# Kernel optimization log

Hardware: AMD Instinct MI355X
Metric: run time of the kernel (lower is better)

Reference implementation:

```python
import jax, jax.numpy as jnp
import numpy as np
from jax import lax

B, T, I, H, L = 64, 256, 512, 1024, 2


def setup_inputs() -> dict:
    key = jax.random.key(0)
    ks = jax.random.split(key, 6)
    s = 0.05  # small init scale for numerical stability
    return {
        "x": jax.random.normal(ks[0], (B, T, I), dtype=jnp.float32),
        "h0": jnp.zeros((L, B, H), dtype=jnp.float32),
        "c0": jnp.zeros((L, B, H), dtype=jnp.float32),
        "W_ih_0": jax.random.normal(ks[1], (I, 4 * H), dtype=jnp.float32) * s,
        "W_hh_0": jax.random.normal(ks[2], (H, 4 * H), dtype=jnp.float32) * s,
        "b_0": jnp.zeros((4 * H,), dtype=jnp.float32),
        "W_ih_1": jax.random.normal(ks[3], (H, 4 * H), dtype=jnp.float32) * s,
        "W_hh_1": jax.random.normal(ks[4], (H, 4 * H), dtype=jnp.float32) * s,
        "b_1": jnp.zeros((4 * H,), dtype=jnp.float32),
    }


def _lstm_layer(x_tbd, h0, c0, W_ih, W_hh, b):
    """x_tbd: [T, B, in]; returns ([T, B, H], h_T, c_T). Standard (Zaremba) LSTM cell."""
    def step(carry, xt):
        h, c = carry
        gates = xt @ W_ih + h @ W_hh + b  # [B, 4H]
        i, f, g, o = jnp.split(gates, 4, axis=-1)
        i = jax.nn.sigmoid(i)
        f = jax.nn.sigmoid(f)
        g = jnp.tanh(g)
        o = jax.nn.sigmoid(o)
        c_new = f * c + i * g
        h_new = o * jnp.tanh(c_new)
        return (h_new, c_new), h_new

    (h_T, c_T), ys = lax.scan(step, (h0, c0), x_tbd)
    return ys, h_T, c_T


def reference(x, h0, c0, W_ih_0, W_hh_0, b_0, W_ih_1, W_hh_1, b_1):
    # x: [B, T, I] batch-first as in the torch module; scan over time.
    xt = jnp.swapaxes(x, 0, 1)  # [T, B, I]
    weights = [(W_ih_0, W_hh_0, b_0), (W_ih_1, W_hh_1, b_1)]
    hs, cs = [], []
    values = xt
    for l in range(L):
        W_ih, W_hh, b = weights[l]
        values, h_T, c_T = _lstm_layer(values, h0[l], c0[l], W_ih, W_hh, b)
        hs.append(h_T)
        cs.append(c_T)
    outputs = jnp.swapaxes(values, 0, 1)  # [B, T, H]
    return outputs, jnp.stack(hs, 0), jnp.stack(cs, 0)
```

## Files before the change

kernel.cpp:

```cpp
#include <hip/hip_runtime.h>
#include <hip/hip_bf16.h>

typedef __attribute__((ext_vector_type(8))) short short8;
typedef __attribute__((ext_vector_type(4))) float f32x4;

constexpr int BB = 64;
constexpr int TT = 256;
constexpr int II = 512;
constexpr int HH = 1024;

constexpr int NBLK = 256;
constexpr int NTHR = 512;

constexpr int HTILE = (HH / 8) * BB * 8;
constexpr int XTILE = (II / 8) * BB * 8;

constexpr size_t OFF_FLAGS = 0;
constexpr size_t OFF_WIH0T = 4096;
constexpr size_t OFF_WHH0T = OFF_WIH0T + (size_t)4096 * 512 * 2;
constexpr size_t OFF_WIH1T = OFF_WHH0T + (size_t)4096 * 1024 * 2;
constexpr size_t OFF_WHH1T = OFF_WIH1T + (size_t)4096 * 1024 * 2;
constexpr size_t OFF_XT    = OFF_WHH1T + (size_t)4096 * 1024 * 2;
constexpr size_t OFF_H0D   = OFF_XT + (size_t)TT * XTILE * 2;
constexpr size_t OFF_H1D   = OFF_H0D + (size_t)4 * HTILE * 2;

__device__ __forceinline__ float sigmoid_(float x) {
  return 1.f / (1.f + __expf(-x));
}
__device__ __forceinline__ float tanh_(float x) {
  float ax = fabsf(x);
  float e = __expf(-2.f * ax);
  float t = (1.f - e) / (1.f + e);
  return copysignf(t, x);
}

__global__ void zero_flags(int* f) { f[blockIdx.x * 256 + threadIdx.x] = 0; }

__global__ void transpose_to_bf16(const float* __restrict__ src,
                                  __hip_bfloat16* __restrict__ dst,
                                  int K, int N) {
  __shared__ float tile[64][65];
  const int n0 = blockIdx.x * 64;
  const int k0 = blockIdx.y * 64;
  const int tx = threadIdx.x & 63;
  const int ty = threadIdx.x >> 6;
#pragma unroll
  for (int i = 0; i < 64; i += 4)
    tile[ty + i][tx] = src[(size_t)(k0 + ty + i) * N + n0 + tx];
  __syncthreads();
#pragma unroll
  for (int i = 0; i < 64; i += 4) {
    const int n = ty + i;
    dst[(size_t)(n0 + n) * K + k0 + tx] = __float2bfloat16(tile[tx][n]);
  }
}

__global__ void tile_x(const float* __restrict__ x, __hip_bfloat16* __restrict__ xt) {
  const int t = blockIdx.x;
  const int k = threadIdx.x;
  __hip_bfloat16* o = xt + (size_t)t * XTILE;
  for (int b = 0; b < BB; ++b) {
    float v = x[((size_t)b * TT + t) * II + k];
    o[(k >> 3) * (BB * 8) + b * 8 + (k & 7)] = __float2bfloat16(v);
  }
}

__global__ void init_h(const float* __restrict__ h0, __hip_bfloat16* h0d, __hip_bfloat16* h1d) {
  const int idx = blockIdx.x * 256 + threadIdx.x;
  const int l = idx >> 16;
  const int b = (idx >> 10) & 63;
  const int j = idx & 1023;
  __hip_bfloat16 v = __float2bfloat16(h0[idx]);
  __hip_bfloat16* dst = l ? h1d : h0d;
  dst[(j >> 3) * (BB * 8) + b * 8 + (j & 7)] = v;
}

template <int KI, int KW, int LAYER>
__device__ __forceinline__ void scan_impl(
    const __hip_bfloat16* __restrict__ xsrc,
    const __hip_bfloat16* __restrict__ WiT,
    const __hip_bfloat16* __restrict__ WhT,
    const float* __restrict__ bias,
    const float* __restrict__ c0_in,
    __hip_bfloat16* h0d, __hip_bfloat16* h1d,
    float* __restrict__ out, int* flags, float (*part)[2][4][4][65],
    int bhalf, int jbase, bool leader) {
  const int tid = threadIdx.x;
  const int wave = tid >> 6;
  const int lane = tid & 63;
  const int cc = lane & 15;
  const int lrow = lane >> 4;

  const int kbase = wave * (KW * 32);

  short8 Bf[KW][4];
#pragma unroll
  for (int w = 0; w < KW; ++w) {
    const int kg = kbase + w * 32 + lrow * 8;
#pragma unroll
    for (int g = 0; g < 4; ++g) {
      const int gcol = g * HH + jbase + cc;
      const __hip_bfloat16* p;
      if (kg < KI) p = WiT + (size_t)gcol * KI + kg;
      else         p = WhT + (size_t)gcol * HH + (kg - KI);
      Bf[w][g] = *(const short8*)p;
    }
  }

  const int ejl = tid & 15;
  const int ebl = tid >> 4;
  const int ej = jbase + ejl;
  const int eb = bhalf * 32 + ebl;
  const int pm = ebl >> 4, psub = (ebl >> 2) & 3, pr = ebl & 3;
  const int plane = psub * 16 + ejl;
  const float bi = bias[ej];
  const float bf_ = bias[HH + ej];
  const float bg = bias[2 * HH + ej];
  const float bo = bias[3 * HH + ej];
  float cst = c0_in[(size_t)LAYER * BB * HH + (size_t)eb * HH + ej];

  for (int tau = 0; tau <= TT; ++tau) {
    if (tau > 0 && wave == 0) {
      for (;;) {
        int v0 = __hip_atomic_load(&flags[lane],       __ATOMIC_RELAXED, __HIP_MEMORY_SCOPE_AGENT);
        int v1 = __hip_atomic_load(&flags[lane + 64],  __ATOMIC_RELAXED, __HIP_MEMORY_SCOPE_AGENT);
        int v2 = __hip_atomic_load(&flags[lane + 128], __ATOMIC_RELAXED, __HIP_MEMORY_SCOPE_AGENT);
        int v3 = __hip_atomic_load(&flags[lane + 192], __ATOMIC_RELAXED, __HIP_MEMORY_SCOPE_AGENT);
        int mn = min(min(v0, v1), min(v2, v3));
        if (__all(mn >= tau)) break;
        __builtin_amdgcn_s_sleep(2);
      }
    }
    __syncthreads();
    asm volatile("s_waitcnt vmcnt(0)" ::: "memory");
    if (leader && wave == 0)
      __builtin_amdgcn_fence(__ATOMIC_ACQUIRE, "agent");
    asm volatile("buffer_inv sc0" ::: "memory");
    __builtin_amdgcn_sched_barrier(0);

    const bool active = (LAYER == 0) ? (tau < TT) : (tau >= 1);
    if (active) {
      const int p = (LAYER == 0) ? tau : tau - 1;
      const __hip_bfloat16* px;
      const __hip_bfloat16* ph;
      __hip_bfloat16* hout;
      if constexpr (LAYER == 0) {
        px = xsrc + (size_t)p * XTILE;
        ph = h0d + (size_t)(p & 3) * HTILE;
        hout = h0d + (size_t)((p + 1) & 3) * HTILE;
      } else {
        px = h0d + (size_t)((p + 1) & 3) * HTILE;
        ph = h1d + (size_t)(p & 3) * HTILE;
        hout = h1d + (size_t)((p + 1) & 3) * HTILE;
      }

      f32x4 acc[2][4] = {};
      short8 abuf[4][2];

      auto issue_pair = [&](int w, short8* dst) {
        const int kg = kbase + w * 32;
        const __hip_bfloat16* ab;
        int kc;
        bool hpath;
        if (kg < KI) { ab = px; kc = (kg >> 3) + lrow; hpath = (LAYER == 1); }
        else         { ab = ph; kc = ((kg - KI) >> 3) + lrow; hpath = true; }
#pragma unroll
        for (int m = 0; m < 2; ++m) {
          const __hip_bfloat16* ptr =
              ab + (size_t)kc * (BB * 8) + (size_t)(bhalf * 32 + m * 16 + cc) * 8;
          if (hpath)
            asm volatile("global_load_dwordx4 %0, %1, off sc0" : "=v"(dst[m]) : "v"(ptr));
          else
            asm volatile("global_load_dwordx4 %0, %1, off" : "=v"(dst[m]) : "v"(ptr));
        }
      };

#pragma unroll
      for (int w = 0; w < 4; ++w) issue_pair(w, abuf[w]);

#pragma unroll
      for (int w = 0; w < KW; ++w) {
        const int op = (KW - w < 4) ? (KW - w) : 4;
        const int vm = 2 * (op - 1);
        if (vm == 6)      asm volatile("s_waitcnt vmcnt(6)" ::: "memory");
        else if (vm == 4) asm volatile("s_waitcnt vmcnt(4)" ::: "memory");
        else if (vm == 2) asm volatile("s_waitcnt vmcnt(2)" ::: "memory");
        else              asm volatile("s_waitcnt vmcnt(0)" ::: "memory");
        __builtin_amdgcn_sched_barrier(0);
#pragma unroll
        for (int m = 0; m < 2; ++m)
#pragma unroll
          for (int g = 0; g < 4; ++g)
            acc[m][g] = __builtin_amdgcn_mfma_f32_16x16x32_bf16(
                abuf[w & 3][m], Bf[w][g], acc[m][g], 0, 0, 0);
        if (w + 4 < KW) issue_pair(w + 4, abuf[w & 3]);
      }

#pragma unroll
      for (int m = 0; m < 2; ++m)
#pragma unroll
        for (int g = 0; g < 4; ++g)
#pragma unroll
          for (int r = 0; r < 4; ++r)
            part[wave][m][g][r][lane] = acc[m][g][r];
      __syncthreads();

      float s0 = 0.f, s1 = 0.f, s2 = 0.f, s3 = 0.f;
#pragma unroll
      for (int w = 0; w < 8; ++w) {
        s0 += part[w][pm][0][pr][plane];
        s1 += part[w][pm][1][pr][plane];
        s2 += part[w][pm][2][pr][plane];
        s3 += part[w][pm][3][pr][plane];
      }
      float iv = sigmoid_(s0 + bi);
      float fv = sigmoid_(s1 + bf_);
      float gv = tanh_(s2 + bg);
      float ov = sigmoid_(s3 + bo);
      float cn = fv * cst + iv * gv;
      cst = cn;
      float hv = ov * tanh_(cn);
      __hip_bfloat16 hb = __float2bfloat16(hv);
      unsigned short hu = *reinterpret_cast<unsigned short*>(&hb);
      unsigned pu = (unsigned)__shfl_xor((int)hu, 1);
      if ((tid & 1) == 0) {
        uint32_t packed = (uint32_t)hu | ((pu & 0xffffu) << 16);
        uint32_t* hq = (uint32_t*)hout;
        __hip_atomic_store(hq + (ej >> 3) * 256 + eb * 4 + ((ej & 7) >> 1), packed,
                           __ATOMIC_RELAXED, __HIP_MEMORY_SCOPE_AGENT);
      }
      asm volatile("s_waitcnt vmcnt(0)" ::: "memory");
      __syncthreads();
      if (tid == 0)
        __hip_atomic_store(&flags[blockIdx.x], tau + 1, __ATOMIC_RELAXED, __HIP_MEMORY_SCOPE_AGENT);
      if constexpr (LAYER == 1)
        out[((size_t)eb * TT + p) * HH + ej] = hv;
      if (p == TT - 1) {
        out[(size_t)BB * TT * HH + (size_t)LAYER * BB * HH + (size_t)eb * HH + ej] = hv;
        out[(size_t)BB * TT * HH + (size_t)2 * BB * HH + (size_t)LAYER * BB * HH + (size_t)eb * HH + ej] = cn;
      }
    } else {
      __syncthreads();
      if (tid == 0)
        __hip_atomic_store(&flags[blockIdx.x], tau + 1, __ATOMIC_RELAXED, __HIP_MEMORY_SCOPE_AGENT);
    }
  }
}

__global__ __launch_bounds__(NTHR, 2) void lstm_scan(
    const __hip_bfloat16* __restrict__ xt,
    const __hip_bfloat16* __restrict__ Wih0T, const __hip_bfloat16* __restrict__ Whh0T,
    const __hip_bfloat16* __restrict__ Wih1T, const __hip_bfloat16* __restrict__ Whh1T,
    const float* __restrict__ b0, const float* __restrict__ b1,
    const float* __restrict__ c0_in,
    __hip_bfloat16* h0d, __hip_bfloat16* h1d,
    float* __restrict__ out, int* flags) {
  __shared__ float part[8][2][4][4][65];
  __shared__ int s_leader;
  if (threadIdx.x == 0) {
    unsigned xcd;
    asm volatile("s_getreg_b32 %0, hwreg(HW_REG_XCC_ID)" : "=s"(xcd));
    int t = __hip_atomic_fetch_add(&flags[256 + (xcd & 15)], 1,
                                   __ATOMIC_RELAXED, __HIP_MEMORY_SCOPE_AGENT);
    s_leader = (t == 0);
  }
  __syncthreads();
  const bool leader = (s_leader != 0);

  const int blk = blockIdx.x;
  const int jslot = blk & 63;
  const int bhalf = (blk >> 6) & 1;
  const int jbase = jslot * 16;
  if ((blk >> 7) == 0)
    scan_impl<512, 6, 0>(xt, Wih0T, Whh0T, b0, c0_in, h0d, h1d, out, flags, part, bhalf, jbase, leader);
  else
    scan_impl<1024, 8, 1>(nullptr, Wih1T, Whh1T, b1, c0_in, h0d, h1d, out, flags, part, bhalf, jbase, leader);
}

extern "C" void kernel_launch(void* const* d_in, const int* in_sizes, int n_in,
                              void* d_out, int out_size, void* d_ws, size_t ws_size,
                              hipStream_t stream) {
  (void)in_sizes; (void)n_in; (void)out_size; (void)ws_size;
  const float* x    = (const float*)d_in[0];
  const float* h0   = (const float*)d_in[1];
  const float* c0   = (const float*)d_in[2];
  const float* Wih0 = (const float*)d_in[3];
  const float* Whh0 = (const float*)d_in[4];
  const float* b0   = (const float*)d_in[5];
  const float* Wih1 = (const float*)d_in[6];
  const float* Whh1 = (const float*)d_in[7];
  const float* b1   = (const float*)d_in[8];
  float* out = (float*)d_out;
  char* ws = (char*)d_ws;

  int* flags = (int*)(ws + OFF_FLAGS);
  __hip_bfloat16* wih0t = (__hip_bfloat16*)(ws + OFF_WIH0T);
  __hip_bfloat16* whh0t = (__hip_bfloat16*)(ws + OFF_WHH0T);
  __hip_bfloat16* wih1t = (__hip_bfloat16*)(ws + OFF_WIH1T);
  __hip_bfloat16* whh1t = (__hip_bfloat16*)(ws + OFF_WHH1T);
  __hip_bfloat16* xtl   = (__hip_bfloat16*)(ws + OFF_XT);
  __hip_bfloat16* h0d   = (__hip_bfloat16*)(ws + OFF_H0D);
  __hip_bfloat16* h1d   = (__hip_bfloat16*)(ws + OFF_H1D);

  zero_flags<<<2, 256, 0, stream>>>(flags);
  transpose_to_bf16<<<dim3(64, 8),  256, 0, stream>>>(Wih0, wih0t, 512, 4096);
  transpose_to_bf16<<<dim3(64, 16), 256, 0, stream>>>(Whh0, whh0t, 1024, 4096);
  transpose_to_bf16<<<dim3(64, 16), 256, 0, stream>>>(Wih1, wih1t, 1024, 4096);
  transpose_to_bf16<<<dim3(64, 16), 256, 0, stream>>>(Whh1, whh1t, 1024, 4096);
  tile_x<<<TT, 512, 0, stream>>>(x, xtl);
  init_h<<<512, 256, 0, stream>>>(h0, h0d, h1d);
  lstm_scan<<<NBLK, NTHR, 0, stream>>>(xtl, wih0t, whh0t, wih1t, whh1t,
                                       b0, b1, c0, h0d, h1d, out, flags);
}
```

Before: 1.682 ms.

## Prefetch and compute dependency-free GEMM chunks before the per-step flag wait

Reorders each wave's K chunks so that the part of the gate GEMM not depending on the current step's recurrent state is loaded and multiplied before spinning on the inter-block flags. For layer 0 that part is the x input; for layer 1 it is the layer-0 output. Layer 1 now lags layer 0 by two steps and the h ring grows from 4 to 8 slots so that input is already published. It also drops the per-XCD leader election and explicit buffer_inv and sc0 loads, using an agent-scope acquire fence from wave 0 in every block instead. Hiding the input half of the GEMM behind the barrier latency targets the serial critical path. The costs are one extra pipeline step, an extra __syncthreads per step, and reliance on the fence alone for cache coherence.

After: 1.618 ms. 3.8% less time.

```diff
diff --git a/kernel.cpp b/kernel.cpp
--- a/kernel.cpp
+++ b/kernel.cpp
@@ -14,6 +14,7 @@
 
 constexpr int HTILE = (HH / 8) * BB * 8;
 constexpr int XTILE = (II / 8) * BB * 8;
+constexpr int RING = 8;
 
 constexpr size_t OFF_FLAGS = 0;
 constexpr size_t OFF_WIH0T = 4096;
@@ -22,7 +23,7 @@
 constexpr size_t OFF_WHH1T = OFF_WIH1T + (size_t)4096 * 1024 * 2;
 constexpr size_t OFF_XT    = OFF_WHH1T + (size_t)4096 * 1024 * 2;
 constexpr size_t OFF_H0D   = OFF_XT + (size_t)TT * XTILE * 2;
-constexpr size_t OFF_H1D   = OFF_H0D + (size_t)4 * HTILE * 2;
+constexpr size_t OFF_H1D   = OFF_H0D + (size_t)RING * HTILE * 2;
 
 __device__ __forceinline__ float sigmoid_(float x) {
   return 1.f / (1.f + __expf(-x));
@@ -75,7 +76,15 @@
   dst[(j >> 3) * (BB * 8) + b * 8 + (j & 7)] = v;
 }
 
-template <int KI, int KW, int LAYER>
+template <int LAYER>
+__device__ __forceinline__ int chunk_kg(int wave, int c) {
+  if constexpr (LAYER == 0)
+    return (c < 2) ? (wave * 2 + c) * 32 : 512 + (wave * 4 + (c - 2)) * 32;
+  else
+    return (c < 4) ? (wave * 4 + c) * 32 : 1024 + (wave * 4 + (c - 4)) * 32;
+}
+
+template <int KI, int KW, int CA, int LAYER>
 __device__ __forceinline__ void scan_impl(
     const __hip_bfloat16* __restrict__ xsrc,
     const __hip_bfloat16* __restrict__ WiT,
@@ -84,26 +93,24 @@
     const float* __restrict__ c0_in,
     __hip_bfloat16* h0d, __hip_bfloat16* h1d,
     float* __restrict__ out, int* flags, float (*part)[2][4][4][65],
-    int bhalf, int jbase, bool leader) {
+    int bhalf, int jbase) {
   const int tid = threadIdx.x;
   const int wave = tid >> 6;
   const int lane = tid & 63;
   const int cc = lane & 15;
   const int lrow = lane >> 4;
 
-  const int kbase = wave * (KW * 32);
-
   short8 Bf[KW][4];
 #pragma unroll
-  for (int w = 0; w < KW; ++w) {
-    const int kg = kbase + w * 32 + lrow * 8;
+  for (int c = 0; c < KW; ++c) {
+    const int kg = chunk_kg<LAYER>(wave, c) + lrow * 8;
 #pragma unroll
     for (int g = 0; g < 4; ++g) {
       const int gcol = g * HH + jbase + cc;
       const __hip_bfloat16* p;
       if (kg < KI) p = WiT + (size_t)gcol * KI + kg;
       else         p = WhT + (size_t)gcol * HH + (kg - KI);
-      Bf[w][g] = *(const short8*)p;
+      Bf[c][g] = *(const short8*)p;
     }
   }
 
@@ -119,7 +126,45 @@
   const float bo = bias[3 * HH + ej];
   float cst = c0_in[(size_t)LAYER * BB * HH + (size_t)eb * HH + ej];
 
-  for (int tau = 0; tau <= TT; ++tau) {
+  for (int tau = 0; tau < TT + 2; ++tau) {
+    const bool active = (LAYER == 0) ? (tau < TT) : (tau >= 2);
+    const int p = (LAYER == 0) ? tau : tau - 2;
+
+    const __hip_bfloat16* px;
+    const __hip_bfloat16* ph;
+    __hip_bfloat16* hout;
+    if constexpr (LAYER == 0) {
+      px = xsrc + (size_t)p * XTILE;
+      ph = h0d + (size_t)(p & (RING - 1)) * HTILE;
+      hout = h0d + (size_t)((p + 1) & (RING - 1)) * HTILE;
+    } else {
+      px = h0d + (size_t)((p + 1) & (RING - 1)) * HTILE;
+      ph = h1d + (size_t)(p & (RING - 1)) * HTILE;
+      hout = h1d + (size_t)((p + 1) & (RING - 1)) * HTILE;
+    }
+
+    f32x4 acc[2][4] = {};
+    short8 abuf[4][2];
+
+    auto issue_chunk = [&](int c, short8* dst) {
+      const int kg = chunk_kg<LAYER>(wave, c);
+      const __hip_bfloat16* ab;
+      int kc;
+      if (kg < KI) { ab = px; kc = (kg >> 3) + lrow; }
+      else         { ab = ph; kc = ((kg - KI) >> 3) + lrow; }
+#pragma unroll
+      for (int m = 0; m < 2; ++m) {
+        const __hip_bfloat16* ptr =
+            ab + (size_t)kc * (BB * 8) + (size_t)(bhalf * 32 + m * 16 + cc) * 8;
+        asm volatile("global_load_dwordx4 %0, %1, off" : "=v"(dst[m]) : "v"(ptr));
+      }
+    };
+
+    if (active) {
+#pragma unroll
+      for (int c = 0; c < CA; ++c) issue_chunk(c, abuf[c]);
+    }
+
     if (tau > 0 && wave == 0) {
       for (;;) {
         int v0 = __hip_atomic_load(&flags[lane],       __ATOMIC_RELAXED, __HIP_MEMORY_SCOPE_AGENT);
@@ -131,57 +176,32 @@
         __builtin_amdgcn_s_sleep(2);
       }
     }
+
+    if (active) {
+      asm volatile("s_waitcnt vmcnt(0)" ::: "memory");
+      __builtin_amdgcn_sched_barrier(0);
+#pragma unroll
+      for (int c = 0; c < CA; ++c)
+#pragma unroll
+        for (int m = 0; m < 2; ++m)
+#pragma unroll
+          for (int g = 0; g < 4; ++g)
+            acc[m][g] = __builtin_amdgcn_mfma_f32_16x16x32_bf16(
+                abuf[c][m], Bf[c][g], acc[m][g], 0, 0, 0);
+    }
+
     __syncthreads();
-    asm volatile("s_waitcnt vmcnt(0)" ::: "memory");
-    if (leader && wave == 0)
+    if (wave == 0)
       __builtin_amdgcn_fence(__ATOMIC_ACQUIRE, "agent");
-    asm volatile("buffer_inv sc0" ::: "memory");
-    __builtin_amdgcn_sched_barrier(0);
-
-    const bool active = (LAYER == 0) ? (tau < TT) : (tau >= 1);
+    __syncthreads();
+
     if (active) {
-      const int p = (LAYER == 0) ? tau : tau - 1;
-      const __hip_bfloat16* px;
-      const __hip_bfloat16* ph;
-      __hip_bfloat16* hout;
-      if constexpr (LAYER == 0) {
-        px = xsrc + (size_t)p * XTILE;
-        ph = h0d + (size_t)(p & 3) * HTILE;
-        hout = h0d + (size_t)((p + 1) & 3) * HTILE;
-      } else {
-        px = h0d + (size_t)((p + 1) & 3) * HTILE;
-        ph = h1d + (size_t)(p & 3) * HTILE;
-        hout = h1d + (size_t)((p + 1) & 3) * HTILE;
-      }
-
-      f32x4 acc[2][4] = {};
-      short8 abuf[4][2];
-
-      auto issue_pair = [&](int w, short8* dst) {
-        const int kg = kbase + w * 32;
-        const __hip_bfloat16* ab;
-        int kc;
-        bool hpath;
-        if (kg < KI) { ab = px; kc = (kg >> 3) + lrow; hpath = (LAYER == 1); }
-        else         { ab = ph; kc = ((kg - KI) >> 3) + lrow; hpath = true; }
-#pragma unroll
-        for (int m = 0; m < 2; ++m) {
-          const __hip_bfloat16* ptr =
-              ab + (size_t)kc * (BB * 8) + (size_t)(bhalf * 32 + m * 16 + cc) * 8;
-          if (hpath)
-            asm volatile("global_load_dwordx4 %0, %1, off sc0" : "=v"(dst[m]) : "v"(ptr));
-          else
-            asm volatile("global_load_dwordx4 %0, %1, off" : "=v"(dst[m]) : "v"(ptr));
-        }
-      };
-
-#pragma unroll
-      for (int w = 0; w < 4; ++w) issue_pair(w, abuf[w]);
-
-#pragma unroll
-      for (int w = 0; w < KW; ++w) {
-        const int op = (KW - w < 4) ? (KW - w) : 4;
-        const int vm = 2 * (op - 1);
+      constexpr int NB = KW - CA;
+#pragma unroll
+      for (int c = 0; c < NB; ++c) issue_chunk(CA + c, abuf[c]);
+#pragma unroll
+      for (int c = 0; c < NB; ++c) {
+        const int vm = 2 * (NB - 1 - c);
         if (vm == 6)      asm volatile("s_waitcnt vmcnt(6)" ::: "memory");
         else if (vm == 4) asm volatile("s_waitcnt vmcnt(4)" ::: "memory");
         else if (vm == 2) asm volatile("s_waitcnt vmcnt(2)" ::: "memory");
@@ -192,8 +212,7 @@
 #pragma unroll
           for (int g = 0; g < 4; ++g)
             acc[m][g] = __builtin_amdgcn_mfma_f32_16x16x32_bf16(
-                abuf[w & 3][m], Bf[w][g], acc[m][g], 0, 0, 0);
-        if (w + 4 < KW) issue_pair(w + 4, abuf[w & 3]);
+                abuf[c][m], Bf[CA + c][g], acc[m][g], 0, 0, 0);
       }
 
 #pragma unroll
@@ -256,25 +275,14 @@
     __hip_bfloat16* h0d, __hip_bfloat16* h1d,
     float* __restrict__ out, int* flags) {
   __shared__ float part[8][2][4][4][65];
-  __shared__ int s_leader;
-  if (threadIdx.x == 0) {
-    unsigned xcd;
-    asm volatile("s_getreg_b32 %0, hwreg(HW_REG_XCC_ID)" : "=s"(xcd));
-    int t = __hip_atomic_fetch_add(&flags[256 + (xcd & 15)], 1,
-                                   __ATOMIC_RELAXED, __HIP_MEMORY_SCOPE_AGENT);
-    s_leader = (t == 0);
-  }
-  __syncthreads();
-  const bool leader = (s_leader != 0);
-
   const int blk = blockIdx.x;
   const int jslot = blk & 63;
   const int bhalf = (blk >> 6) & 1;
   const int jbase = jslot * 16;
   if ((blk >> 7) == 0)
-    scan_impl<512, 6, 0>(xt, Wih0T, Whh0T, b0, c0_in, h0d, h1d, out, flags, part, bhalf, jbase, leader);
+    scan_impl<512, 6, 2, 0>(xt, Wih0T, Whh0T, b0, c0_in, h0d, h1d, out, flags, part, bhalf, jbase);
   else
-    scan_impl<1024, 8, 1>(nullptr, Wih1T, Whh1T, b1, c0_in, h0d, h1d, out, flags, part, bhalf, jbase, leader);
+    scan_impl<1024, 8, 4, 1>(nullptr, Wih1T, Whh1T, b1, c0_in, h0d, h1d, out, flags, part, bhalf, jbase);
 }
 
 extern "C" void kernel_launch(void* const* d_in, const int* in_sizes, int n_in,
```
